# Optimization experiments

Hardware: AMD Instinct MI355X
Metric: run time of the kernel (lower is better)

The kernel has to match this reference:

```python
import jax, jax.numpy as jnp
import numpy as np

B, C, D, H, W = 2, 64, 3, 96, 96
CD = C * D  # conv1x1 channel count = in_dim * 3


def setup_inputs() -> dict:
    key = jax.random.key(0)
    ks = jax.random.split(key, 7)
    s = 1.0 / np.sqrt(CD)
    x = jax.random.normal(ks[0], (B, C, D, H, W), dtype=jnp.float32)
    Wq = jax.random.uniform(ks[1], (CD, CD), jnp.float32, -s, s)
    bq = jax.random.uniform(ks[2], (CD,), jnp.float32, -s, s)
    Wk = jax.random.uniform(ks[3], (CD, CD), jnp.float32, -s, s)
    bk = jax.random.uniform(ks[4], (CD,), jnp.float32, -s, s)
    Wv = jax.random.uniform(ks[5], (CD, CD), jnp.float32, -s, s)
    bv = jax.random.uniform(ks[6], (CD,), jnp.float32, -s, s)
    return {"x": x, "Wq": Wq, "bq": bq, "Wk": Wk, "bk": bk, "Wv": Wv, "bv": bv}


def reference(x, Wq, bq, Wk, bk, Wv, bv):
    b, c, d, h, w = x.shape
    n = h * w
    xr = x.reshape(b, c * d, n)  # [B, CD, N]; conv1x1 == channel matmul
    q = jnp.einsum('oc,bcn->bon', Wq, xr) + bq[:, None]  # [B, CD, N]
    k = jnp.einsum('oc,bcn->bon', Wk, xr) + bk[:, None]
    v = jnp.einsum('oc,bcn->bon', Wv, xr) + bv[:, None]
    energy = jnp.einsum('bcn,bcm->bnm', q, k)            # [B, N, N]
    attention = jax.nn.softmax(energy, axis=-1)
    # out = bmm(value, attention^T): out[b,c,m] = sum_n v[b,c,n] * attn[b,m,n]
    out = jnp.einsum('bcn,bmn->bcm', v, attention)       # [B, CD, N]
    return out.reshape(b, c, d, h, w)
```

## Files before the change

kernel.cpp:

```cpp
#include <hip/hip_runtime.h>

#define NSEQ  9216
#define CDIM  192
#define KTILE 64
#define LOG2E 1.44269504088896f

typedef _Float16 h8_t  __attribute__((ext_vector_type(8)));
typedef _Float16 h4_t  __attribute__((ext_vector_type(4)));
typedef _Float16 h2_t  __attribute__((ext_vector_type(2)));
typedef float    f4_t  __attribute__((ext_vector_type(4)));
typedef float    f16v  __attribute__((ext_vector_type(16)));

__global__ __launch_bounds__(256) void wconv_kernel(
    const float* __restrict__ Wq, const float* __restrict__ Wk,
    const float* __restrict__ Wv, _Float16* __restrict__ Wh)
{
    int i = blockIdx.x * 256 + threadIdx.x;
    if (i >= 3 * 9216) return;
    const float* src = (i < 9216) ? Wq : (i < 18432 ? Wk : Wv);
    float s = (i < 9216) ? LOG2E : 1.f;
    int r = i % 9216;
    f4_t w = ((const f4_t*)src)[r];
    h4_t h = {(_Float16)(w[0]*s), (_Float16)(w[1]*s),
              (_Float16)(w[2]*s), (_Float16)(w[3]*s)};
    ((h4_t*)Wh)[i] = h;
}

__global__ __launch_bounds__(256) void proj_kernel(
    const float* __restrict__ x, const _Float16* __restrict__ Wh,
    const float* __restrict__ bq, const float* __restrict__ bk,
    const float* __restrict__ bv,
    _Float16* __restrict__ QT, _Float16* __restrict__ KT, _Float16* __restrict__ Vg)
{
    const int tid  = threadIdx.x;
    const int lane = tid & 63, wave = tid >> 6;
    const int L31  = lane & 31, hi = lane >> 5;
    const int idx  = blockIdx.x * 4 + wave;
    const int mat  = idx / 1152;
    const int rem  = idx % 1152;
    const int half = rem / 576;
    const int rem2 = rem % 576;
    const int b    = rem2 / 288;
    const int n0   = (rem2 % 288) * 32;
    const int n    = n0 + L31;

    h8_t bf[12];
    #pragma unroll
    for (int t = 0; t < 12; t++) {
        h8_t h;
        #pragma unroll
        for (int j = 0; j < 8; j++)
            h[j] = (_Float16)x[(size_t)(b * CDIM + t * 16 + hi * 8 + j) * NSEQ + n];
        bf[t] = h;
    }

    const _Float16* W = Wh + mat * CDIM * CDIM + half * 96 * CDIM;
    const float* bias = ((mat == 0) ? bq : (mat == 1 ? bk : bv)) + half * 96;
    const float bscale = (mat == 0) ? LOG2E : 1.f;

    f16v acc[3];
    #pragma unroll
    for (int s = 0; s < 3; s++)
        #pragma unroll
        for (int r = 0; r < 16; r++) acc[s][r] = 0.f;

    #pragma unroll
    for (int t = 0; t < 12; t++) {
        #pragma unroll
        for (int s = 0; s < 3; s++) {
            h8_t a = *(const h8_t*)(W + (s * 32 + L31) * CDIM + t * 16 + hi * 8);
            acc[s] = __builtin_amdgcn_mfma_f32_32x32x16_f16(a, bf[t], acc[s], 0, 0, 0);
        }
    }

    if (mat < 2) {
        _Float16* dst = ((mat == 0) ? QT : KT)
                        + ((size_t)b * NSEQ + n) * CDIM + half * 96;
        #pragma unroll
        for (int s = 0; s < 3; s++) {
            #pragma unroll
            for (int g = 0; g < 4; g++) {
                f4_t bb = *(const f4_t*)&bias[s * 32 + 8 * g + 4 * hi];
                h4_t h = {(_Float16)(acc[s][4*g+0] + bb[0] * bscale),
                          (_Float16)(acc[s][4*g+1] + bb[1] * bscale),
                          (_Float16)(acc[s][4*g+2] + bb[2] * bscale),
                          (_Float16)(acc[s][4*g+3] + bb[3] * bscale)};
                *(h4_t*)(dst + s * 32 + 8 * g + 4 * hi) = h;
            }
        }
    } else {
        #pragma unroll
        for (int s = 0; s < 3; s++) {
            #pragma unroll
            for (int g = 0; g < 4; g++) {
                f4_t bb = *(const f4_t*)&bias[s * 32 + 8 * g + 4 * hi];
                #pragma unroll
                for (int r = 0; r < 4; r++) {
                    int o = half * 96 + s * 32 + 8 * g + 4 * hi + r;
                    Vg[((size_t)b * CDIM + o) * NSEQ + n] =
                        (_Float16)(acc[s][4*g+r] + bb[r]);
                }
            }
        }
    }
}

template<int NSPLIT>
__global__ __launch_bounds__(256, 2) void flash_kernel(
    const _Float16* __restrict__ QT, const _Float16* __restrict__ KTg,
    const _Float16* __restrict__ Vg,
    _Float16* __restrict__ O_part, float* __restrict__ m_part, float* __restrict__ l_part)
{
    constexpr int KPS    = NSEQ / NSPLIT;
    constexpr int KITERS = KPS / KTILE;

    __shared__ __align__(16) _Float16 K_s[KTILE * 200];
    __shared__ __align__(16) _Float16 V_s[CDIM * 72];
    __shared__ __align__(16) _Float16 P_s[4 * 32 * 72];
    __shared__ float alpha_s[4][32];

    const int tid  = threadIdx.x;
    const int lane = tid & 63, wave = tid >> 6;
    const int L31  = lane & 31, hi = lane >> 5;
    const int qtile = blockIdx.x, split = blockIdx.y, b = blockIdx.z;
    const int q0 = qtile * 128 + wave * 32;

    h8_t qf[12];
    const _Float16* qbase = QT + ((size_t)b * NSEQ + q0 + L31) * CDIM + hi * 8;
    #pragma unroll
    for (int t = 0; t < 12; t++) qf[t] = *(const h8_t*)(qbase + t * 16);

    f16v acc[6];
    #pragma unroll
    for (int s = 0; s < 6; s++)
        #pragma unroll
        for (int r = 0; r < 16; r++) acc[s][r] = 0.f;
    float m_run = -__builtin_inff();
    float l_run = 0.f;

    const _Float16* ksrc = KTg + ((size_t)b * NSEQ + split * KPS) * CDIM;
    const _Float16* vsrc = Vg + (size_t)b * CDIM * NSEQ + split * KPS;

    for (int kt = 0; kt < KITERS; kt++) {
        __syncthreads();
        {
            const h8_t* src = (const h8_t*)(ksrc + (size_t)kt * KTILE * CDIM);
            #pragma unroll
            for (int t = 0; t < 6; t++) {
                int i = tid + t * 256;
                int row = i / 24, col = i % 24;
                *(h8_t*)(K_s + row * 200 + col * 8) = src[i];
            }
            #pragma unroll
            for (int t = 0; t < 6; t++) {
                int i = tid + t * 256;
                int c = i >> 3, seg = i & 7;
                *(h8_t*)(V_s + c * 72 + seg * 8) =
                    *(const h8_t*)(vsrc + (size_t)c * NSEQ + kt * KTILE + seg * 8);
            }
        }
        __syncthreads();

        f16v st[2];
        #pragma unroll
        for (int s = 0; s < 2; s++)
            #pragma unroll
            for (int r = 0; r < 16; r++) st[s][r] = 0.f;
        #pragma unroll
        for (int t = 0; t < 12; t++) {
            #pragma unroll
            for (int s = 0; s < 2; s++) {
                h8_t a = *(const h8_t*)(K_s + (s * 32 + L31) * 200 + t * 16 + hi * 8);
                st[s] = __builtin_amdgcn_mfma_f32_32x32x16_f16(a, qf[t], st[s], 0, 0, 0);
            }
        }

        float mx = fmaxf(st[0][0], st[1][0]);
        #pragma unroll
        for (int r = 1; r < 16; r++) mx = fmaxf(mx, fmaxf(st[0][r], st[1][r]));
        mx = fmaxf(mx, __shfl_xor(mx, 32));
        float m_new = fmaxf(m_run, mx);

        float p[32];
        float psum = 0.f;
        #pragma unroll
        for (int s = 0; s < 2; s++)
            #pragma unroll
            for (int r = 0; r < 16; r++) {
                float e = __builtin_exp2f(st[s][r] - m_new);
                p[s * 16 + r] = e;
                psum += e;
            }

        if (__any(m_new > m_run)) {
            float alpha = __builtin_exp2f(m_run - m_new);
            l_run = l_run * alpha + psum;
            if (lane < 32) alpha_s[wave][lane] = alpha;
            __asm__ volatile("" ::: "memory");
            f4_t a4[4];
            #pragma unroll
            for (int g = 0; g < 4; g++)
                a4[g] = *(const f4_t*)&alpha_s[wave][8 * g + 4 * hi];
            #pragma unroll
            for (int cs = 0; cs < 6; cs++)
                #pragma unroll
                for (int r = 0; r < 16; r++) acc[cs][r] *= a4[r >> 2][r & 3];
        } else {
            l_run += psum;
        }
        m_run = m_new;

        _Float16* prow = P_s + wave * 32 * 72 + L31 * 72;
        #pragma unroll
        for (int s = 0; s < 2; s++)
            #pragma unroll
            for (int g = 0; g < 4; g++) {
                h4_t h = {(_Float16)p[s*16+4*g+0], (_Float16)p[s*16+4*g+1],
                          (_Float16)p[s*16+4*g+2], (_Float16)p[s*16+4*g+3]};
                *(h4_t*)(prow + s * 32 + 8 * g + 4 * hi) = h;
            }
        __asm__ volatile("" ::: "memory");

        #pragma unroll
        for (int ks = 0; ks < 4; ks++) {
            h8_t pa = *(const h8_t*)(prow + ks * 16 + hi * 8);
            #pragma unroll
            for (int cs = 0; cs < 6; cs++) {
                h8_t vb = *(const h8_t*)(V_s + (cs * 32 + L31) * 72 + ks * 16 + hi * 8);
                acc[cs] = __builtin_amdgcn_mfma_f32_32x32x16_f16(pa, vb, acc[cs], 0, 0, 0);
            }
        }
    }

    float l_tot = l_run + __shfl_xor(l_run, 32);
    const size_t pbase = (size_t)(b * NSPLIT + split) * NSEQ + q0;
    if (lane < 32) {
        m_part[pbase + lane] = m_run;
        l_part[pbase + lane] = l_tot;
    }
    _Float16* obase = O_part + pbase * CDIM;
    #pragma unroll
    for (int cs = 0; cs < 6; cs++)
        #pragma unroll
        for (int r = 0; r < 16; r++) {
            int q = (r & 3) + 8 * (r >> 2) + 4 * hi;
            obase[(size_t)q * CDIM + cs * 32 + L31] = (_Float16)acc[cs][r];
        }
}

template<int NS>
__global__ __launch_bounds__(256) void combine_kernel(
    const _Float16* __restrict__ O_part, const float* __restrict__ m_part,
    const float* __restrict__ l_part, float* __restrict__ out)
{
    __shared__ float Cs[CDIM][65];
    __shared__ float winv[NS][64];
    const int tid = threadIdx.x;
    const int b  = blockIdx.y;
    const int n0 = blockIdx.x * 64;

    if (tid < 64) {
        int n = n0 + tid;
        float mm[NS], ll[NS], ms = -__builtin_inff();
        #pragma unroll
        for (int s = 0; s < NS; s++) {
            mm[s] = m_part[(b * NS + s) * NSEQ + n];
            ll[s] = l_part[(b * NS + s) * NSEQ + n];
            ms = fmaxf(ms, mm[s]);
        }
        float denom = 0.f;
        #pragma unroll
        for (int s = 0; s < NS; s++) {
            float w = __builtin_exp2f(mm[s] - ms);
            mm[s] = w;
            denom += w * ll[s];
        }
        #pragma unroll
        for (int s = 0; s < NS; s++) winv[s][tid] = mm[s] / denom;
    }
    __syncthreads();

    for (int i = tid; i < 64 * 48; i += 256) {
        int nl = i / 48, c4 = i % 48;
        float v0 = 0.f, v1 = 0.f, v2 = 0.f, v3 = 0.f;
        #pragma unroll
        for (int s = 0; s < NS; s++) {
            h4_t op = *(const h4_t*)(O_part +
                ((size_t)(b * NS + s) * NSEQ + n0 + nl) * CDIM + c4 * 4);
            float w = winv[s][nl];
            v0 += w * (float)op[0];
            v1 += w * (float)op[1];
            v2 += w * (float)op[2];
            v3 += w * (float)op[3];
        }
        Cs[c4 * 4 + 0][nl] = v0;
        Cs[c4 * 4 + 1][nl] = v1;
        Cs[c4 * 4 + 2][nl] = v2;
        Cs[c4 * 4 + 3][nl] = v3;
    }
    __syncthreads();
    for (int i = tid; i < CDIM * 64; i += 256) {
        int nl = i & 63, c = i >> 6;
        out[((size_t)b * CDIM + c) * NSEQ + n0 + nl] = Cs[c][nl];
    }
}

extern "C" void kernel_launch(void* const* d_in, const int* in_sizes, int n_in,
                              void* d_out, int out_size, void* d_ws, size_t ws_size,
                              hipStream_t stream)
{
    const float* x  = (const float*)d_in[0];
    const float* Wq = (const float*)d_in[1];
    const float* bq = (const float*)d_in[2];
    const float* Wk = (const float*)d_in[3];
    const float* bk = (const float*)d_in[4];
    const float* Wv = (const float*)d_in[5];
    const float* bv = (const float*)d_in[6];
    float* out = (float*)d_out;

    char* ws = (char*)d_ws;
    _Float16* QT = (_Float16*)(ws);
    _Float16* KT = (_Float16*)(ws + 7077888);
    _Float16* Vg = (_Float16*)(ws + 14155776);
    char* tail = ws + 21233664;
    _Float16* Wh = (_Float16*)tail;
    _Float16* O_part = (_Float16*)tail;

    wconv_kernel<<<108, 256, 0, stream>>>(Wq, Wk, Wv, Wh);
    proj_kernel<<<864, 256, 0, stream>>>(x, Wh, bq, bk, bv, QT, KT, Vg);

    const size_t need8 = 21233664ull + 8 * 7077888ull + 2 * 589824ull;
    const size_t need4 = 21233664ull + 4 * 7077888ull + 2 * 294912ull;
    if (ws_size >= need8) {
        float* m_part = (float*)(tail + 8 * 7077888ull);
        float* l_part = (float*)(tail + 8 * 7077888ull + 589824ull);
        flash_kernel<8><<<dim3(72, 8, 2), 256, 0, stream>>>(QT, KT, Vg, O_part, m_part, l_part);
        combine_kernel<8><<<dim3(144, 2), 256, 0, stream>>>(O_part, m_part, l_part, out);
    } else if (ws_size >= need4) {
        float* m_part = (float*)(tail + 4 * 7077888ull);
        float* l_part = (float*)(tail + 4 * 7077888ull + 294912ull);
        flash_kernel<4><<<dim3(72, 4, 2), 256, 0, stream>>>(QT, KT, Vg, O_part, m_part, l_part);
        combine_kernel<4><<<dim3(144, 2), 256, 0, stream>>>(O_part, m_part, l_part, out);
    } else {
        float* m_part = (float*)(tail + 2 * 7077888ull);
        float* l_part = (float*)(tail + 2 * 7077888ull + 147456ull);
        flash_kernel<2><<<dim3(72, 2, 2), 256, 0, stream>>>(QT, KT, Vg, O_part, m_part, l_part);
        combine_kernel<2><<<dim3(144, 2), 256, 0, stream>>>(O_part, m_part, l_part, out);
    }
}
```

Baseline: 305.0 us.

## Pre-swizzle K into MFMA fragment layout and stream it directly from global

The projection kernel now writes K in a per-32-row MFMA-fragment layout, so each lane of the flash kernel can load its A operand straight from global memory with a two-deep register prefetch. This removes the K shared-memory tile and its staging stores. V is now prefetched into registers one tile ahead, overlapping the global loads with compute. Max and sum reductions use tree form for more ILP. The cost is that every wave reloads the K fragments from global/L2 rather than sharing them through LDS, and register pressure goes up.

Measured after the change: 341.4 us. +12.0%, slower.

```diff
diff --git a/kernel.cpp b/kernel.cpp
--- a/kernel.cpp
+++ b/kernel.cpp
@@ -30,7 +30,7 @@
     const float* __restrict__ x, const _Float16* __restrict__ Wh,
     const float* __restrict__ bq, const float* __restrict__ bk,
     const float* __restrict__ bv,
-    _Float16* __restrict__ QT, _Float16* __restrict__ KT, _Float16* __restrict__ Vg)
+    _Float16* __restrict__ QT, _Float16* __restrict__ KF, _Float16* __restrict__ Vg)
 {
     const int tid  = threadIdx.x;
     const int lane = tid & 63, wave = tid >> 6;
@@ -73,9 +73,8 @@
         }
     }
 
-    if (mat < 2) {
-        _Float16* dst = ((mat == 0) ? QT : KT)
-                        + ((size_t)b * NSEQ + n) * CDIM + half * 96;
+    if (mat == 0) {
+        _Float16* dst = QT + ((size_t)b * NSEQ + n) * CDIM + half * 96;
         #pragma unroll
         for (int s = 0; s < 3; s++) {
             #pragma unroll
@@ -86,6 +85,22 @@
                           (_Float16)(acc[s][4*g+2] + bb[2] * bscale),
                           (_Float16)(acc[s][4*g+3] + bb[3] * bscale)};
                 *(h4_t*)(dst + s * 32 + 8 * g + 4 * hi) = h;
+            }
+        }
+    } else if (mat == 1) {
+        _Float16* kf = KF + (size_t)b * (288 * 6144) + (size_t)(n0 >> 5) * 6144;
+        #pragma unroll
+        for (int s = 0; s < 3; s++) {
+            #pragma unroll
+            for (int g = 0; g < 4; g++) {
+                f4_t bb = *(const f4_t*)&bias[s * 32 + 8 * g + 4 * hi];
+                h4_t h = {(_Float16)(acc[s][4*g+0] + bb[0]),
+                          (_Float16)(acc[s][4*g+1] + bb[1]),
+                          (_Float16)(acc[s][4*g+2] + bb[2]),
+                          (_Float16)(acc[s][4*g+3] + bb[3])};
+                int t   = half * 6 + 2 * s + (g >> 1);
+                int hif = g & 1;
+                *(h4_t*)(kf + (t * 2 + hif) * 256 + L31 * 8 + 4 * hi) = h;
             }
         }
     } else {
@@ -107,14 +122,13 @@
 
 template<int NSPLIT>
 __global__ __launch_bounds__(256, 2) void flash_kernel(
-    const _Float16* __restrict__ QT, const _Float16* __restrict__ KTg,
+    const _Float16* __restrict__ QT, const _Float16* __restrict__ KF,
     const _Float16* __restrict__ Vg,
     _Float16* __restrict__ O_part, float* __restrict__ m_part, float* __restrict__ l_part)
 {
     constexpr int KPS    = NSEQ / NSPLIT;
     constexpr int KITERS = KPS / KTILE;
 
-    __shared__ __align__(16) _Float16 K_s[KTILE * 200];
     __shared__ __align__(16) _Float16 V_s[CDIM * 72];
     __shared__ __align__(16) _Float16 P_s[4 * 32 * 72];
     __shared__ float alpha_s[4][32];
@@ -138,28 +152,40 @@
     float m_run = -__builtin_inff();
     float l_run = 0.f;
 
-    const _Float16* ksrc = KTg + ((size_t)b * NSEQ + split * KPS) * CDIM;
+    const _Float16* kfb = KF + (size_t)b * (288 * 6144)
+                        + (size_t)(split * (KPS / 32)) * 6144 + (size_t)lane * 8;
     const _Float16* vsrc = Vg + (size_t)b * CDIM * NSEQ + split * KPS;
 
+    const _Float16* vgl[6];
+    _Float16*       vds[6];
+    #pragma unroll
+    for (int r = 0; r < 6; r++) {
+        int i = r * 256 + tid;
+        int c = i >> 3, seg = i & 7;
+        vgl[r] = vsrc + (size_t)c * NSEQ + seg * 8;
+        vds[r] = V_s + c * 72 + seg * 8;
+    }
+    h8_t vreg[6];
+    #pragma unroll
+    for (int r = 0; r < 6; r++) vreg[r] = *(const h8_t*)(vgl[r]);
+
     for (int kt = 0; kt < KITERS; kt++) {
+        const _Float16* kf0 = kfb + (size_t)(kt * 2) * 6144;
+        const _Float16* kf1 = kf0 + 6144;
+        h8_t cur0 = *(const h8_t*)(kf0);
+        h8_t cur1 = *(const h8_t*)(kf1);
+        h8_t nxt0 = *(const h8_t*)(kf0 + 512);
+        h8_t nxt1 = *(const h8_t*)(kf1 + 512);
+
         __syncthreads();
-        {
-            const h8_t* src = (const h8_t*)(ksrc + (size_t)kt * KTILE * CDIM);
-            #pragma unroll
-            for (int t = 0; t < 6; t++) {
-                int i = tid + t * 256;
-                int row = i / 24, col = i % 24;
-                *(h8_t*)(K_s + row * 200 + col * 8) = src[i];
-            }
-            #pragma unroll
-            for (int t = 0; t < 6; t++) {
-                int i = tid + t * 256;
-                int c = i >> 3, seg = i & 7;
-                *(h8_t*)(V_s + c * 72 + seg * 8) =
-                    *(const h8_t*)(vsrc + (size_t)c * NSEQ + kt * KTILE + seg * 8);
-            }
-        }
+        #pragma unroll
+        for (int r = 0; r < 6; r++) *(h8_t*)(vds[r]) = vreg[r];
         __syncthreads();
+        if (kt + 1 < KITERS) {
+            #pragma unroll
+            for (int r = 0; r < 6; r++)
+                vreg[r] = *(const h8_t*)(vgl[r] + (kt + 1) * KTILE);
+        }
 
         f16v st[2];
         #pragma unroll
@@ -168,29 +194,40 @@
             for (int r = 0; r < 16; r++) st[s][r] = 0.f;
         #pragma unroll
         for (int t = 0; t < 12; t++) {
-            #pragma unroll
-            for (int s = 0; s < 2; s++) {
-                h8_t a = *(const h8_t*)(K_s + (s * 32 + L31) * 200 + t * 16 + hi * 8);
-                st[s] = __builtin_amdgcn_mfma_f32_32x32x16_f16(a, qf[t], st[s], 0, 0, 0);
-            }
-        }
-
-        float mx = fmaxf(st[0][0], st[1][0]);
-        #pragma unroll
-        for (int r = 1; r < 16; r++) mx = fmaxf(mx, fmaxf(st[0][r], st[1][r]));
-        mx = fmaxf(mx, __shfl_xor(mx, 32));
+            h8_t pf0 = nxt0, pf1 = nxt1;
+            if (t + 2 < 12) {
+                pf0 = *(const h8_t*)(kf0 + (t + 2) * 512);
+                pf1 = *(const h8_t*)(kf1 + (t + 2) * 512);
+            }
+            st[0] = __builtin_amdgcn_mfma_f32_32x32x16_f16(cur0, qf[t], st[0], 0, 0, 0);
+            st[1] = __builtin_amdgcn_mfma_f32_32x32x16_f16(cur1, qf[t], st[1], 0, 0, 0);
+            cur0 = nxt0; cur1 = nxt1; nxt0 = pf0; nxt1 = pf1;
+        }
+
+        float v[32];
+        #pragma unroll
+        for (int r = 0; r < 16; r++) { v[r] = st[0][r]; v[16 + r] = st[1][r]; }
+        float mv[32];
+        #pragma unroll
+        for (int r = 0; r < 32; r++) mv[r] = v[r];
+        #pragma unroll
+        for (int w = 16; w >= 1; w >>= 1)
+            #pragma unroll
+            for (int i = 0; i < w; i++) mv[i] = fmaxf(mv[i], mv[i + w]);
+        float mx = fmaxf(mv[0], __shfl_xor(mv[0], 32));
         float m_new = fmaxf(m_run, mx);
 
         float p[32];
-        float psum = 0.f;
-        #pragma unroll
-        for (int s = 0; s < 2; s++)
-            #pragma unroll
-            for (int r = 0; r < 16; r++) {
-                float e = __builtin_exp2f(st[s][r] - m_new);
-                p[s * 16 + r] = e;
-                psum += e;
-            }
+        #pragma unroll
+        for (int r = 0; r < 32; r++) p[r] = __builtin_exp2f(v[r] - m_new);
+        float sv[32];
+        #pragma unroll
+        for (int r = 0; r < 32; r++) sv[r] = p[r];
+        #pragma unroll
+        for (int w = 16; w >= 1; w >>= 1)
+            #pragma unroll
+            for (int i = 0; i < w; i++) sv[i] += sv[i + w];
+        float psum = sv[0];
 
         if (__any(m_new > m_run)) {
             float alpha = __builtin_exp2f(m_run - m_new);
@@ -320,31 +357,31 @@
 
     char* ws = (char*)d_ws;
     _Float16* QT = (_Float16*)(ws);
-    _Float16* KT = (_Float16*)(ws + 7077888);
+    _Float16* KF = (_Float16*)(ws + 7077888);
     _Float16* Vg = (_Float16*)(ws + 14155776);
     char* tail = ws + 21233664;
     _Float16* Wh = (_Float16*)tail;
     _Float16* O_part = (_Float16*)tail;
 
     wconv_kernel<<<108, 256, 0, stream>>>(Wq, Wk, Wv, Wh);
-    proj_kernel<<<864, 256, 0, stream>>>(x, Wh, bq, bk, bv, QT, KT, Vg);
+    proj_kernel<<<864, 256, 0, stream>>>(x, Wh, bq, bk, bv, QT, KF, Vg);
 
     const size_t need8 = 21233664ull + 8 * 7077888ull + 2 * 589824ull;
     const size_t need4 = 21233664ull + 4 * 7077888ull + 2 * 294912ull;
     if (ws_size >= need8) {
         float* m_part = (float*)(tail + 8 * 7077888ull);
         float* l_part = (float*)(tail + 8 * 7077888ull + 589824ull);
-        flash_kernel<8><<<dim3(72, 8, 2), 256, 0, stream>>>(QT, KT, Vg, O_part, m_part, l_part);
+        flash_kernel<8><<<dim3(72, 8, 2), 256, 0, stream>>>(QT, KF, Vg, O_part, m_part, l_part);
         combine_kernel<8><<<dim3(144, 2), 256, 0, stream>>>(O_part, m_part, l_part, out);
     } else if (ws_size >= need4) {
         float* m_part = (float*)(tail + 4 * 7077888ull);
         float* l_part = (float*)(tail + 4 * 7077888ull + 294912ull);
-        flash_kernel<4><<<dim3(72, 4, 2), 256, 0, stream>>>(QT, KT, Vg, O_part, m_part, l_part);
+        flash_kernel<4><<<dim3(72, 4, 2), 256, 0, stream>>>(QT, KF, Vg, O_part, m_part, l_part);
         combine_kernel<4><<<dim3(144, 2), 256, 0, stream>>>(O_part, m_part, l_part, out);
     } else {
         float* m_part = (float*)(tail + 2 * 7077888ull);
         float* l_part = (float*)(tail + 2 * 7077888ull + 147456ull);
-        flash_kernel<2><<<dim3(72, 2, 2), 256, 0, stream>>>(QT, KT, Vg, O_part, m_part, l_part);
+        flash_kernel<2><<<dim3(72, 2, 2), 256, 0, stream>>>(QT, KF, Vg, O_part, m_part, l_part);
         combine_kernel<2><<<dim3(144, 2), 256, 0, stream>>>(O_part, m_part, l_part, out);
     }
 }
```
